# Kernel tuning notes

Hardware: AMD Instinct MI355X
Metric: run time of the kernel (lower is better)

## Reference

```python
import jax, jax.numpy as jnp
import numpy as np

B, H = 32, 1024  # seq_len == hidden_size (required by the original code's shapes)
S = H

def setup_inputs() -> dict:
    key = jax.random.key(0)
    k1, k2, k3, k4, k5 = jax.random.split(key, 5)
    hidden = jax.random.normal(k1, (B, H), dtype=jnp.float32)
    encoder_outputs = jax.random.normal(k2, (B, S, H), dtype=jnp.float32)
    # nn.Linear(2H -> H): weight [H, 2H], bias [H]
    lim = 1.0 / np.sqrt(2 * H)
    W = jax.random.uniform(k3, (H, 2 * H), dtype=jnp.float32, minval=-lim, maxval=lim)
    b = jax.random.uniform(k4, (H,), dtype=jnp.float32, minval=-lim, maxval=lim)
    # v ~ Normal(0, 1/H)
    v = jax.random.normal(k5, (H,), dtype=jnp.float32) * (1.0 / H)
    return {"hidden": hidden, "encoder_outputs": encoder_outputs, "W": W, "b": b, "v": v}

def reference(hidden, encoder_outputs, W, b, v):
    # hidden: [B, H]; encoder_outputs: [B, S, H] with S == H
    S_len = encoder_outputs.shape[1]
    h_rep = jnp.broadcast_to(hidden[:, None, :], (hidden.shape[0], S_len, hidden.shape[1]))
    enc_t = jnp.swapaxes(encoder_outputs, 1, 2)  # [B, H, S] == [B, S, H] (square)
    x = jnp.concatenate([h_rep, enc_t], axis=2)  # [B, S, 2H]
    energy = jnp.tanh(jnp.einsum('bsk,hk->bsh', x, W) + b)  # [B, S, H]
    # scores[b,s] = sum_h v[h] * energy[b,s,h], softmax over s
    scores = jax.nn.softmax(jnp.einsum('h,bsh->bs', v, energy), axis=1)  # [B, S]
    # bmm(scores[B,1,S], enc_t.transpose(1,2)=encoder_outputs[B,S,H]) -> [B, H]
    context = jnp.einsum('bs,bsh->bh', scores, encoder_outputs)
    return context, scores[:, None, :]
```

## Files before the change

kernel.cpp:

```cpp
#include <hip/hip_runtime.h>
#include <hip/hip_bf16.h>
#include <math.h>

#define B_ 32
#define H_ 1024
#define S_ 1024

typedef float  f32x4_t  __attribute__((ext_vector_type(4)));
typedef float  f32x16_t __attribute__((ext_vector_type(16)));
typedef long long i64;
typedef i64 i64x2 __attribute__((ext_vector_type(2)));
typedef unsigned char u8;

__device__ __forceinline__ void gl_lds16(const void* g, void* l) {
    __builtin_amdgcn_global_load_lds(
        (const __attribute__((address_space(1))) unsigned int*)g,
        (__attribute__((address_space(3))) unsigned int*)l, 16, 0, 0);
}

__device__ __forceinline__ float tanh_fast(float x) {
    float e = __builtin_amdgcn_exp2f(x * 2.885390081777927f);
    return 1.f - 2.f * __builtin_amdgcn_rcpf(e + 1.f);
}

__device__ __forceinline__ int kperm(int k) {
    return (k & ~24) | ((k & 8) << 1) | ((k & 16) >> 1);
}

__global__ __launch_bounds__(256) void prep_kernel(
    const float* __restrict__ enc, const float* __restrict__ W,
    const float* __restrict__ hidden, const float* __restrict__ bias,
    u8* __restrict__ encF8, u8* __restrict__ W2f8,
    float* __restrict__ t1, float* __restrict__ logits,
    float* __restrict__ ctx)
{
    __shared__ float T[64 * 65];
    const int idx = blockIdx.x;
    const int tid = threadIdx.x;
    if (idx < 8192) {
        const int b  = idx >> 8;
        const int k0 = ((idx >> 4) & 15) * 64;
        const int s0 = (idx & 15) * 64;
        #pragma unroll
        for (int it = 0; it < 4; ++it) {
            int flat = tid + it * 256;
            int r = flat >> 4, c4 = flat & 15;
            float4 vv = *reinterpret_cast<const float4*>(
                enc + ((size_t)b * S_ + k0 + r) * H_ + s0 + c4 * 4);
            T[r * 65 + c4 * 4 + 0] = vv.x;
            T[r * 65 + c4 * 4 + 1] = vv.y;
            T[r * 65 + c4 * 4 + 2] = vv.z;
            T[r * 65 + c4 * 4 + 3] = vv.w;
        }
        __syncthreads();
        {
            int c   = tid & 1;
            int ktl = (tid >> 1) & 1;
            int s   = tid >> 2;
            int w4[4];
            #pragma unroll
            for (int w = 0; w < 4; ++w) {
                float f[4];
                #pragma unroll
                for (int u = 0; u < 4; ++u) {
                    int i   = w * 4 + u;
                    int k32 = 16 * (i >> 3) + 8 * c + (i & 7);
                    f[u] = T[(ktl * 32 + k32) * 65 + s];
                }
                int pw = __builtin_amdgcn_cvt_pk_fp8_f32(f[0], f[1], 0, false);
                pw     = __builtin_amdgcn_cvt_pk_fp8_f32(f[2], f[3], pw, true);
                w4[w] = pw;
            }
            int4 payload = { w4[0], w4[1], w4[2], w4[3] };
            *reinterpret_cast<int4*>(
                encF8 + (size_t)b * 1048576 + (size_t)((k0 >> 5) + ktl) * 32768
                + (size_t)(s0 + s) * 32 + c * 16) = payload;
        }
    } else if (idx < 9216) {
        int h = idx - 8192;
        if (tid < 64) {
            int z = h * 64 + tid;
            if (z < B_ * S_) logits[z] = 0.f;
            else             ctx[z - B_ * S_] = 0.f;
        }
        int kt = tid >> 3;
        int q  = tid & 7;
        int src = kperm(q * 4);
        float4 wv = *reinterpret_cast<const float4*>(
            W + (size_t)h * (2 * H_) + H_ + kt * 32 + src);
        int pw = __builtin_amdgcn_cvt_pk_fp8_f32(wv.x * 64.f, wv.y * 64.f, 0, false);
        pw     = __builtin_amdgcn_cvt_pk_fp8_f32(wv.z * 64.f, wv.w * 64.f, pw, true);
        *reinterpret_cast<int*>(W2f8 + (size_t)kt * 32768 + (size_t)h * 32 + q * 4) = pw;
    } else {
        int h    = (idx - 9216) * 4 + (tid >> 6);
        int lane = tid & 63;
        const float4* wp = reinterpret_cast<const float4*>(W + (size_t)h * (2 * H_));
        float4 w0 = wp[lane], w1 = wp[lane + 64], w2 = wp[lane + 128], w3 = wp[lane + 192];
        float bh = bias[h];
        for (int b = 0; b < B_; ++b) {
            const float4* hp = reinterpret_cast<const float4*>(hidden + b * H_);
            float4 h0 = hp[lane], h1 = hp[lane + 64], h2 = hp[lane + 128], h3 = hp[lane + 192];
            float a = w0.x*h0.x + w0.y*h0.y + w0.z*h0.z + w0.w*h0.w
                    + w1.x*h1.x + w1.y*h1.y + w1.z*h1.z + w1.w*h1.w
                    + w2.x*h2.x + w2.y*h2.y + w2.z*h2.z + w2.w*h2.w
                    + w3.x*h3.x + w3.y*h3.y + w3.z*h3.z + w3.w*h3.w;
            #pragma unroll
            for (int off = 1; off < 64; off <<= 1) a += __shfl_xor(a, off);
            if (lane == 0) t1[b * H_ + h] = a + bh;
        }
    }
}

__global__ __launch_bounds__(256) void energy_kernel(
    const u8* __restrict__ W2f8, const u8* __restrict__ encF8,
    const float* __restrict__ t1, const float* __restrict__ v,
    float* __restrict__ logits)
{
    __shared__ __align__(16) u8 As[2][4096];
    __shared__ __align__(16) u8 Bs[2][4096];

    const int b     = blockIdx.z;
    const int h0    = blockIdx.x * 128;
    const int s0    = blockIdx.y * 128;
    const int tid   = threadIdx.x;
    const int lane  = tid & 63;
    const int wid   = tid >> 6;
    const int wm    = (wid & 1) * 64;
    const int wn    = (wid >> 1) * 64;
    const int l32   = lane & 31;
    const int khalf = lane >> 5;

    const int rowl = ((lane & 3) << 3) | ((lane >> 2) & 7);
    const int row  = (wid << 5) | rowl;
    const int cch  = lane >> 5;
    const size_t gofsA = (size_t)(h0 + row) * 32 + cch * 16;
    const size_t gofsB = (size_t)b * 1048576 + (size_t)(s0 + row) * 32 + cch * 16;

    gl_lds16(W2f8 + gofsA, &As[0][tid * 16]);
    gl_lds16(encF8 + gofsB, &Bs[0][tid * 16]);
    __syncthreads();

    f32x16_t acc[2][2] = {};
    const int sl  = ((((l32 & 7) << 2) | (l32 >> 3)) | (khalf << 5)) * 16;
    const int wAo = (wm >> 5) * 1024;
    const int wBo = (wn >> 5) * 1024;

    for (int kt = 0; kt < 32; ++kt) {
        const int cur = kt & 1, nxt = cur ^ 1;
        if (kt < 31) {
            gl_lds16(W2f8 + gofsA + (size_t)(kt + 1) * 32768, &As[nxt][tid * 16]);
            gl_lds16(encF8 + gofsB + (size_t)(kt + 1) * 32768, &Bs[nxt][tid * 16]);
        }
        i64x2 a0 = *reinterpret_cast<const i64x2*>(&As[cur][wAo + sl]);
        i64x2 a1 = *reinterpret_cast<const i64x2*>(&As[cur][wAo + 1024 + sl]);
        i64x2 b0 = *reinterpret_cast<const i64x2*>(&Bs[cur][wBo + sl]);
        i64x2 b1 = *reinterpret_cast<const i64x2*>(&Bs[cur][wBo + 1024 + sl]);
        acc[0][0] = __builtin_amdgcn_mfma_f32_32x32x16_fp8_fp8(a0.x, b0.x, acc[0][0], 0, 0, 0);
        acc[0][1] = __builtin_amdgcn_mfma_f32_32x32x16_fp8_fp8(a0.x, b1.x, acc[0][1], 0, 0, 0);
        acc[1][0] = __builtin_amdgcn_mfma_f32_32x32x16_fp8_fp8(a1.x, b0.x, acc[1][0], 0, 0, 0);
        acc[1][1] = __builtin_amdgcn_mfma_f32_32x32x16_fp8_fp8(a1.x, b1.x, acc[1][1], 0, 0, 0);
        acc[0][0] = __builtin_amdgcn_mfma_f32_32x32x16_fp8_fp8(a0.y, b0.y, acc[0][0], 0, 0, 0);
        acc[0][1] = __builtin_amdgcn_mfma_f32_32x32x16_fp8_fp8(a0.y, b1.y, acc[0][1], 0, 0, 0);
        acc[1][0] = __builtin_amdgcn_mfma_f32_32x32x16_fp8_fp8(a1.y, b0.y, acc[1][0], 0, 0, 0);
        acc[1][1] = __builtin_amdgcn_mfma_f32_32x32x16_fp8_fp8(a1.y, b1.y, acc[1][1], 0, 0, 0);
        __syncthreads();
    }

    float pn0 = 0.f, pn1 = 0.f;
    #pragma unroll
    for (int mt = 0; mt < 2; ++mt)
        #pragma unroll
        for (int r = 0; r < 16; ++r) {
            int rr = wm + mt * 32 + (r & 3) + 8 * (r >> 2) + 4 * khalf;
            int h = h0 + rr;
            float tv = t1[b * H_ + h];
            float vv = v[h];
            pn0 += vv * tanh_fast(acc[mt][0][r] * 0.015625f + tv);
            pn1 += vv * tanh_fast(acc[mt][1][r] * 0.015625f + tv);
        }
    pn0 += __shfl_xor(pn0, 32);
    pn1 += __shfl_xor(pn1, 32);
    if (lane < 32) {
        atomicAdd(&logits[(size_t)b * S_ + s0 + wn + l32], pn0);
        atomicAdd(&logits[(size_t)b * S_ + s0 + wn + 32 + l32], pn1);
    }
}

__global__ __launch_bounds__(256) void ctx_kernel(
    const float* __restrict__ enc, const float* __restrict__ logits,
    float* __restrict__ scores, float* __restrict__ ctx)
{
    __shared__ float sc[1024];
    __shared__ float red[8];
    const int b    = blockIdx.y;
    const int s0   = blockIdx.x * 128;
    const int tid  = threadIdx.x;
    const int lane = tid & 63;
    const int w    = tid >> 6;

    float4 lg = *reinterpret_cast<const float4*>(logits + (size_t)b * S_ + tid * 4);
    float mx = fmaxf(fmaxf(lg.x, lg.y), fmaxf(lg.z, lg.w));
    #pragma unroll
    for (int off = 1; off < 64; off <<= 1) mx = fmaxf(mx, __shfl_xor(mx, off));
    if (lane == 0) red[w] = mx;
    __syncthreads();
    mx = fmaxf(fmaxf(red[0], red[1]), fmaxf(red[2], red[3]));
    const float L2E = 1.44269504088896f;
    float e0 = __builtin_amdgcn_exp2f((lg.x - mx) * L2E);
    float e1 = __builtin_amdgcn_exp2f((lg.y - mx) * L2E);
    float e2 = __builtin_amdgcn_exp2f((lg.z - mx) * L2E);
    float e3 = __builtin_amdgcn_exp2f((lg.w - mx) * L2E);
    float s = e0 + e1 + e2 + e3;
    #pragma unroll
    for (int off = 1; off < 64; off <<= 1) s += __shfl_xor(s, off);
    if (lane == 0) red[4 + w] = s;
    __syncthreads();
    float inv = 1.f / (red[4] + red[5] + red[6] + red[7]);
    float4 sv = { e0 * inv, e1 * inv, e2 * inv, e3 * inv };
    *reinterpret_cast<float4*>(&sc[tid * 4]) = sv;
    if (blockIdx.x == 0)
        *reinterpret_cast<float4*>(scores + (size_t)b * S_ + tid * 4) = sv;
    __syncthreads();

    f32x4_t accv = {0.f, 0.f, 0.f, 0.f};
    const float* ebase = enc + ((size_t)b * S_ + s0) * H_ + tid * 4;
    #pragma unroll 4
    for (int si = 0; si < 128; ++si) {
        float wgt = sc[s0 + si];
        float4 ev = *reinterpret_cast<const float4*>(ebase + (size_t)si * H_);
        accv[0] += wgt * ev.x;
        accv[1] += wgt * ev.y;
        accv[2] += wgt * ev.z;
        accv[3] += wgt * ev.w;
    }
    float* cp = ctx + (size_t)b * H_ + tid * 4;
    atomicAdd(cp + 0, accv[0]);
    atomicAdd(cp + 1, accv[1]);
    atomicAdd(cp + 2, accv[2]);
    atomicAdd(cp + 3, accv[3]);
}

extern "C" void kernel_launch(void* const* d_in, const int* in_sizes, int n_in,
                              void* d_out, int out_size, void* d_ws, size_t ws_size,
                              hipStream_t stream)
{
    (void)in_sizes; (void)n_in; (void)out_size; (void)ws_size;
    const float* hidden = (const float*)d_in[0];
    const float* enc    = (const float*)d_in[1];
    const float* W      = (const float*)d_in[2];
    const float* bias   = (const float*)d_in[3];
    const float* v      = (const float*)d_in[4];

    float* out    = (float*)d_out;
    float* ctx    = out;
    float* scores = out + B_ * H_;

    float* logits = (float*)d_ws;
    float* t1     = logits + B_ * S_;
    u8*    W2f8   = (u8*)(t1 + B_ * H_);
    u8*    encF8  = W2f8 + (size_t)H_ * H_;

    prep_kernel<<<dim3(8192 + 1024 + 256), 256, 0, stream>>>(
        enc, W, hidden, bias, encF8, W2f8, t1, logits, ctx);
    energy_kernel<<<dim3(H_ / 128, S_ / 128, B_), 256, 0, stream>>>(
        W2f8, encF8, t1, v, logits);
    ctx_kernel<<<dim3(S_ / 128, B_), 256, 0, stream>>>(enc, logits, scores, ctx);
}
```

Before: 312.9 us.

## Rework enc fp8 transpose, double K-step staging, block swizzle, smaller ctx chunks

The prep kernel drops the LDS transpose tile. Each thread now reads strided columns of enc straight from global memory and packs fp8 for two K-tiles. The energy kernel stages two K-tiles per pipeline stage, halving the barrier count, and uses a 1D grid with a swizzled block-to-(b,h,s) mapping so that blocks sharing an encoder slab run close together. The ctx kernel halves its per-block S chunk to launch more blocks, which adds more atomics. The strided global reads in prep may coalesce worse than the old tiled transpose.

```diff
diff --git a/kernel.cpp b/kernel.cpp
--- a/kernel.cpp
+++ b/kernel.cpp
@@ -34,50 +34,38 @@
     float* __restrict__ t1, float* __restrict__ logits,
     float* __restrict__ ctx)
 {
-    __shared__ float T[64 * 65];
     const int idx = blockIdx.x;
     const int tid = threadIdx.x;
-    if (idx < 8192) {
-        const int b  = idx >> 8;
-        const int k0 = ((idx >> 4) & 15) * 64;
-        const int s0 = (idx & 15) * 64;
+    if (idx < 4096) {
+        const int b   = idx >> 7;
+        const int r   = idx & 127;
+        const int ktp = r >> 3;
+        const int sg  = r & 7;
+        const int s   = sg * 128 + (tid >> 1);
+        const int c   = tid & 1;
+        const float* ebase = enc + (size_t)b * S_ * H_ + s;
+        u8* obase = encF8 + (size_t)b * 1048576 + (size_t)s * 32 + c * 16;
         #pragma unroll
-        for (int it = 0; it < 4; ++it) {
-            int flat = tid + it * 256;
-            int r = flat >> 4, c4 = flat & 15;
-            float4 vv = *reinterpret_cast<const float4*>(
-                enc + ((size_t)b * S_ + k0 + r) * H_ + s0 + c4 * 4);
-            T[r * 65 + c4 * 4 + 0] = vv.x;
-            T[r * 65 + c4 * 4 + 1] = vv.y;
-            T[r * 65 + c4 * 4 + 2] = vv.z;
-            T[r * 65 + c4 * 4 + 3] = vv.w;
-        }
-        __syncthreads();
-        {
-            int c   = tid & 1;
-            int ktl = (tid >> 1) & 1;
-            int s   = tid >> 2;
+        for (int t = 0; t < 2; ++t) {
+            const int kt = ktp * 2 + t;
+            float f[16];
+            #pragma unroll
+            for (int i = 0; i < 16; ++i) {
+                int k = kt * 32 + 16 * (i >> 3) + 8 * c + (i & 7);
+                f[i] = ebase[(size_t)k * H_];
+            }
             int w4[4];
             #pragma unroll
             for (int w = 0; w < 4; ++w) {
-                float f[4];
-                #pragma unroll
-                for (int u = 0; u < 4; ++u) {
-                    int i   = w * 4 + u;
-                    int k32 = 16 * (i >> 3) + 8 * c + (i & 7);
-                    f[u] = T[(ktl * 32 + k32) * 65 + s];
-                }
-                int pw = __builtin_amdgcn_cvt_pk_fp8_f32(f[0], f[1], 0, false);
-                pw     = __builtin_amdgcn_cvt_pk_fp8_f32(f[2], f[3], pw, true);
+                int pw = __builtin_amdgcn_cvt_pk_fp8_f32(f[4*w+0], f[4*w+1], 0, false);
+                pw     = __builtin_amdgcn_cvt_pk_fp8_f32(f[4*w+2], f[4*w+3], pw, true);
                 w4[w] = pw;
             }
             int4 payload = { w4[0], w4[1], w4[2], w4[3] };
-            *reinterpret_cast<int4*>(
-                encF8 + (size_t)b * 1048576 + (size_t)((k0 >> 5) + ktl) * 32768
-                + (size_t)(s0 + s) * 32 + c * 16) = payload;
-        }
-    } else if (idx < 9216) {
-        int h = idx - 8192;
+            *reinterpret_cast<int4*>(obase + (size_t)kt * 32768) = payload;
+        }
+    } else if (idx < 5120) {
+        int h = idx - 4096;
         if (tid < 64) {
             int z = h * 64 + tid;
             if (z < B_ * S_) logits[z] = 0.f;
@@ -92,7 +80,7 @@
         pw     = __builtin_amdgcn_cvt_pk_fp8_f32(wv.z * 64.f, wv.w * 64.f, pw, true);
         *reinterpret_cast<int*>(W2f8 + (size_t)kt * 32768 + (size_t)h * 32 + q * 4) = pw;
     } else {
-        int h    = (idx - 9216) * 4 + (tid >> 6);
+        int h    = (idx - 5120) * 4 + (tid >> 6);
         int lane = tid & 63;
         const float4* wp = reinterpret_cast<const float4*>(W + (size_t)h * (2 * H_));
         float4 w0 = wp[lane], w1 = wp[lane + 64], w2 = wp[lane + 128], w3 = wp[lane + 192];
@@ -116,12 +104,17 @@
     const float* __restrict__ t1, const float* __restrict__ v,
     float* __restrict__ logits)
 {
-    __shared__ __align__(16) u8 As[2][4096];
-    __shared__ __align__(16) u8 Bs[2][4096];
-
-    const int b     = blockIdx.z;
-    const int h0    = blockIdx.x * 128;
-    const int s0    = blockIdx.y * 128;
+    __shared__ __align__(16) u8 As[2][2][4096];
+    __shared__ __align__(16) u8 Bs[2][2][4096];
+
+    const int id = blockIdx.x;
+    const int q  = id >> 3, r = id & 7;
+    const int ht = q & 7;
+    const int g  = r + ((q >> 3) << 3);
+    const int b  = g >> 3;
+    const int h0 = ht * 128;
+    const int s0 = (g & 7) * 128;
+
     const int tid   = threadIdx.x;
     const int lane  = tid & 63;
     const int wid   = tid >> 6;
@@ -136,8 +129,10 @@
     const size_t gofsA = (size_t)(h0 + row) * 32 + cch * 16;
     const size_t gofsB = (size_t)b * 1048576 + (size_t)(s0 + row) * 32 + cch * 16;
 
-    gl_lds16(W2f8 + gofsA, &As[0][tid * 16]);
-    gl_lds16(encF8 + gofsB, &Bs[0][tid * 16]);
+    gl_lds16(W2f8 + gofsA,          &As[0][0][tid * 16]);
+    gl_lds16(W2f8 + gofsA + 32768,  &As[0][1][tid * 16]);
+    gl_lds16(encF8 + gofsB,         &Bs[0][0][tid * 16]);
+    gl_lds16(encF8 + gofsB + 32768, &Bs[0][1][tid * 16]);
     __syncthreads();
 
     f32x16_t acc[2][2] = {};
@@ -145,24 +140,30 @@
     const int wAo = (wm >> 5) * 1024;
     const int wBo = (wn >> 5) * 1024;
 
-    for (int kt = 0; kt < 32; ++kt) {
-        const int cur = kt & 1, nxt = cur ^ 1;
-        if (kt < 31) {
-            gl_lds16(W2f8 + gofsA + (size_t)(kt + 1) * 32768, &As[nxt][tid * 16]);
-            gl_lds16(encF8 + gofsB + (size_t)(kt + 1) * 32768, &Bs[nxt][tid * 16]);
-        }
-        i64x2 a0 = *reinterpret_cast<const i64x2*>(&As[cur][wAo + sl]);
-        i64x2 a1 = *reinterpret_cast<const i64x2*>(&As[cur][wAo + 1024 + sl]);
-        i64x2 b0 = *reinterpret_cast<const i64x2*>(&Bs[cur][wBo + sl]);
-        i64x2 b1 = *reinterpret_cast<const i64x2*>(&Bs[cur][wBo + 1024 + sl]);
-        acc[0][0] = __builtin_amdgcn_mfma_f32_32x32x16_fp8_fp8(a0.x, b0.x, acc[0][0], 0, 0, 0);
-        acc[0][1] = __builtin_amdgcn_mfma_f32_32x32x16_fp8_fp8(a0.x, b1.x, acc[0][1], 0, 0, 0);
-        acc[1][0] = __builtin_amdgcn_mfma_f32_32x32x16_fp8_fp8(a1.x, b0.x, acc[1][0], 0, 0, 0);
-        acc[1][1] = __builtin_amdgcn_mfma_f32_32x32x16_fp8_fp8(a1.x, b1.x, acc[1][1], 0, 0, 0);
-        acc[0][0] = __builtin_amdgcn_mfma_f32_32x32x16_fp8_fp8(a0.y, b0.y, acc[0][0], 0, 0, 0);
-        acc[0][1] = __builtin_amdgcn_mfma_f32_32x32x16_fp8_fp8(a0.y, b1.y, acc[0][1], 0, 0, 0);
-        acc[1][0] = __builtin_amdgcn_mfma_f32_32x32x16_fp8_fp8(a1.y, b0.y, acc[1][0], 0, 0, 0);
-        acc[1][1] = __builtin_amdgcn_mfma_f32_32x32x16_fp8_fp8(a1.y, b1.y, acc[1][1], 0, 0, 0);
+    for (int seg = 0; seg < 16; ++seg) {
+        const int cur = seg & 1, nxt = cur ^ 1;
+        if (seg < 15) {
+            const size_t o = (size_t)(2 * seg + 2) * 32768;
+            gl_lds16(W2f8 + gofsA + o,          &As[nxt][0][tid * 16]);
+            gl_lds16(W2f8 + gofsA + o + 32768,  &As[nxt][1][tid * 16]);
+            gl_lds16(encF8 + gofsB + o,         &Bs[nxt][0][tid * 16]);
+            gl_lds16(encF8 + gofsB + o + 32768, &Bs[nxt][1][tid * 16]);
+        }
+        #pragma unroll
+        for (int t = 0; t < 2; ++t) {
+            i64x2 a0 = *reinterpret_cast<const i64x2*>(&As[cur][t][wAo + sl]);
+            i64x2 a1 = *reinterpret_cast<const i64x2*>(&As[cur][t][wAo + 1024 + sl]);
+            i64x2 b0 = *reinterpret_cast<const i64x2*>(&Bs[cur][t][wBo + sl]);
+            i64x2 b1 = *reinterpret_cast<const i64x2*>(&Bs[cur][t][wBo + 1024 + sl]);
+            acc[0][0] = __builtin_amdgcn_mfma_f32_32x32x16_fp8_fp8(a0.x, b0.x, acc[0][0], 0, 0, 0);
+            acc[0][1] = __builtin_amdgcn_mfma_f32_32x32x16_fp8_fp8(a0.x, b1.x, acc[0][1], 0, 0, 0);
+            acc[1][0] = __builtin_amdgcn_mfma_f32_32x32x16_fp8_fp8(a1.x, b0.x, acc[1][0], 0, 0, 0);
+            acc[1][1] = __builtin_amdgcn_mfma_f32_32x32x16_fp8_fp8(a1.x, b1.x, acc[1][1], 0, 0, 0);
+            acc[0][0] = __builtin_amdgcn_mfma_f32_32x32x16_fp8_fp8(a0.y, b0.y, acc[0][0], 0, 0, 0);
+            acc[0][1] = __builtin_amdgcn_mfma_f32_32x32x16_fp8_fp8(a0.y, b1.y, acc[0][1], 0, 0, 0);
+            acc[1][0] = __builtin_amdgcn_mfma_f32_32x32x16_fp8_fp8(a1.y, b0.y, acc[1][0], 0, 0, 0);
+            acc[1][1] = __builtin_amdgcn_mfma_f32_32x32x16_fp8_fp8(a1.y, b1.y, acc[1][1], 0, 0, 0);
+        }
         __syncthreads();
     }
 
@@ -170,13 +171,13 @@
     #pragma unroll
     for (int mt = 0; mt < 2; ++mt)
         #pragma unroll
-        for (int r = 0; r < 16; ++r) {
-            int rr = wm + mt * 32 + (r & 3) + 8 * (r >> 2) + 4 * khalf;
-            int h = h0 + rr;
+        for (int rr = 0; rr < 16; ++rr) {
+            int rowm = wm + mt * 32 + (rr & 3) + 8 * (rr >> 2) + 4 * khalf;
+            int h = h0 + rowm;
             float tv = t1[b * H_ + h];
             float vv = v[h];
-            pn0 += vv * tanh_fast(acc[mt][0][r] * 0.015625f + tv);
-            pn1 += vv * tanh_fast(acc[mt][1][r] * 0.015625f + tv);
+            pn0 += vv * tanh_fast(acc[mt][0][rr] * 0.015625f + tv);
+            pn1 += vv * tanh_fast(acc[mt][1][rr] * 0.015625f + tv);
         }
     pn0 += __shfl_xor(pn0, 32);
     pn1 += __shfl_xor(pn1, 32);
@@ -193,7 +194,7 @@
     __shared__ float sc[1024];
     __shared__ float red[8];
     const int b    = blockIdx.y;
-    const int s0   = blockIdx.x * 128;
+    const int s0   = blockIdx.x * 64;
     const int tid  = threadIdx.x;
     const int lane = tid & 63;
     const int w    = tid >> 6;
@@ -225,7 +226,7 @@
     f32x4_t accv = {0.f, 0.f, 0.f, 0.f};
     const float* ebase = enc + ((size_t)b * S_ + s0) * H_ + tid * 4;
     #pragma unroll 4
-    for (int si = 0; si < 128; ++si) {
+    for (int si = 0; si < 64; ++si) {
         float wgt = sc[s0 + si];
         float4 ev = *reinterpret_cast<const float4*>(ebase + (size_t)si * H_);
         accv[0] += wgt * ev.x;
@@ -260,9 +261,8 @@
     u8*    W2f8   = (u8*)(t1 + B_ * H_);
     u8*    encF8  = W2f8 + (size_t)H_ * H_;
 
-    prep_kernel<<<dim3(8192 + 1024 + 256), 256, 0, stream>>>(
+    prep_kernel<<<dim3(4096 + 1024 + 256), 256, 0, stream>>>(
         enc, W, hidden, bias, encF8, W2f8, t1, logits, ctx);
-    energy_kernel<<<dim3(H_ / 128, S_ / 128, B_), 256, 0, stream>>>(
-        W2f8, encF8, t1, v, logits);
-    ctx_kernel<<<dim3(S_ / 128, B_), 256, 0, stream>>>(enc, logits, scores, ctx);
-}
+    energy_kernel<<<dim3(2048), 256, 0, stream>>>(W2f8, encF8, t1, v, logits);
+    ctx_kernel<<<dim3(S_ / 64, B_), 256, 0, stream>>>(enc, logits, scores, ctx);
+}
```

Result: no change. 317.3 us (+1.4%).
